# Performance work log

Hardware: AMD Instinct MI355X
Metric: run time of the kernel (lower is better)

Reference implementation:

```python
import jax, jax.numpy as jnp
import numpy as np

B, H, S, D = 2, 16, 2048, 64
NEG_BIG = -1e30  # stand-in for -inf; exp underflows to 0 identically in fp32


def setup_inputs() -> dict:
    key = jax.random.key(0)
    kq, kk, kv = jax.random.split(key, 3)
    q = jax.random.normal(kq, (B, H, S, D), dtype=jnp.float32)
    k = jax.random.normal(kk, (B, H, S, D), dtype=jnp.float32)
    v = jax.random.normal(kv, (B, H, S, D), dtype=jnp.float32)
    # causal mask, True = attend (matches masked_fill_(mask.logical_not(), -inf))
    mask = jnp.tril(jnp.ones((S, S), dtype=bool))[None, None]  # [1,1,S,S]
    return {"q": q, "k": k, "v": v, "mask": mask}


def reference(q, k, v, mask):
    # scaled dot-product attention: softmax(q k^T / sqrt(d)) v
    scale = q.shape[-1] ** -0.5
    weight = jnp.einsum("bhqd,bhkd->bhqk", q * scale, k)  # [B,H,S,S]
    weight = jnp.where(mask, weight, NEG_BIG)
    score = jax.nn.softmax(weight, axis=-1)  # stable: single max-subtract
    attn = jnp.einsum("bhqk,bhkd->bhqd", score, v)  # [B,H,S,D]
    return attn
```

## Files before the change

### kernel.cpp

```cpp
#include <hip/hip_runtime.h>

#define S_ 2048
#define D_ 64

typedef __bf16 bf16x2v __attribute__((ext_vector_type(2)));
typedef __bf16 bf16x8 __attribute__((ext_vector_type(8)));
typedef float f32x2 __attribute__((ext_vector_type(2)));
typedef float f32x4 __attribute__((ext_vector_type(4)));
typedef float f32x16 __attribute__((ext_vector_type(16)));
typedef unsigned uint4v __attribute__((ext_vector_type(4)));

#define QSCALE 0.180336880f

__device__ __forceinline__ unsigned cvtpk(float lo, float hi) {
    bf16x2v w; w[0] = (__bf16)lo; w[1] = (__bf16)hi;
    return __builtin_bit_cast(unsigned, w);
}

__device__ __forceinline__ float fexp2(float x) { return __builtin_amdgcn_exp2f(x); }

__device__ __forceinline__ int kap(int r) {
    return (r & ~12) | ((r & 4) << 1) | ((r & 8) >> 1);
}

__global__ __launch_bounds__(512, 2)
void fa_fwd(const float* __restrict__ qg, const float* __restrict__ kg,
            const float* __restrict__ vg, float* __restrict__ og) {
    __shared__ __attribute__((aligned(16))) __bf16 K_lds[2][2][64 * 64];
    __shared__ __attribute__((aligned(16))) __bf16 V_lds[2][2][64 * 64];
    __shared__ __attribute__((aligned(16))) float  mrg[9216];

    const int tid  = threadIdx.x;
    const int lane = tid & 63;
    const int wv   = tid >> 6;
    const int g    = wv >> 2;
    const int wq   = wv & 3;
    const int cq   = lane & 31;
    const int h    = lane >> 5;
    const int up   = wq & 1;

    const int bid = blockIdx.x;
    const int s   = bid >> 5;
    const int bh  = ((bid & 7) << 2) | ((bid >> 3) & 3);

    const size_t base = (size_t)bh * (S_ * D_);
    const float* Q = qg + base;
    const float* K = kg + base;
    const float* V = vg + base;
    float*       O = og + base;

    const int stid = tid & 255;
    const int kk   = stid >> 2;
    const int kd   = (stid & 3) * 16;
    const int vd2  = (stid & 31) * 2;
    const int vk8  = (stid >> 5) * 8;
    const int kp   = (kk & 32) | kap(kk & 31);
    const unsigned swq = (unsigned)((cq & 7) << 4);
    const int slot = (wq * 64 + lane) * 36;

    f32x4 rk[4];
    f32x2 rv2[8];

    auto loadtile = [&](int t) {
        const int kv0 = t * 64;
        const float* Kp = K + (size_t)(kv0 + kk) * D_ + kd;
        #pragma unroll
        for (int i = 0; i < 4; ++i) rk[i] = *(const f32x4*)(Kp + 4 * i);
        const float* Vp = V + (size_t)(kv0 + vk8) * D_ + vd2;
        #pragma unroll
        for (int i = 0; i < 8; ++i) rv2[i] = *(const f32x2*)(Vp + (size_t)i * D_);
    };

    auto writetile = [&](int buf) {
        const unsigned swzk = (unsigned)((kp & 7) << 4);
        bf16x8 w0, w1;
        #pragma unroll
        for (int j = 0; j < 4; ++j) {
            w0[j]     = (__bf16)rk[0][j];
            w0[4 + j] = (__bf16)rk[1][j];
            w1[j]     = (__bf16)rk[2][j];
            w1[4 + j] = (__bf16)rk[3][j];
        }
        *(bf16x8*)(&K_lds[g][buf][kp * 64 + ((((unsigned)(2 * kd)) ^ swzk) >> 1)])      = w0;
        *(bf16x8*)(&K_lds[g][buf][kp * 64 + ((((unsigned)(2 * kd + 16)) ^ swzk) >> 1)]) = w1;
        #pragma unroll
        for (int j = 0; j < 2; ++j) {
            const int d = vd2 + j;
            bf16x8 wt;
            #pragma unroll
            for (int i = 0; i < 8; ++i) wt[i] = (__bf16)rv2[i][j];
            *(bf16x8*)(&V_lds[g][buf][d * 64 + ((((unsigned)(2 * vk8)) ^ ((unsigned)((d & 7) << 4))) >> 1)]) = wt;
        }
    };

    for (int pass = 0; pass < 2; ++pass) {
        const int qt    = pass ? s : (15 - s);
        const int q0w   = qt * 128 + wq * 32;
        const int tdiag = 2 * qt + (wq >> 1);
        const int tbase = g ? (qt + 1) : 0;
        const int niter = qt + 1;

        bf16x8 qf[4];
        {
            const float* Qr = Q + (size_t)(q0w + cq) * D_;
            #pragma unroll
            for (int c = 0; c < 4; ++c) {
                const int d0 = c * 16 + h * 8;
                f32x4 a = *(const f32x4*)(Qr + d0);
                f32x4 b = *(const f32x4*)(Qr + d0 + 4);
                bf16x8 f;
                #pragma unroll
                for (int j = 0; j < 4; ++j) {
                    f[j]     = (__bf16)(a[j] * QSCALE);
                    f[4 + j] = (__bf16)(b[j] * QSCALE);
                }
                qf[c] = f;
            }
        }

        f32x16 acc0, acc1;
        #pragma unroll
        for (int i = 0; i < 16; ++i) { acc0[i] = 0.f; acc1[i] = 0.f; }
        float l_r = 0.f;

        auto compute = [&](int t, int buf) {
            const bool diag  = (t == tdiag);
            const bool do_s1 = !diag || up;
            const bool mask0 = diag && !up;
            const bool mask1 = diag && up;

            f32x16 s0, s1;
            #pragma unroll
            for (int i = 0; i < 16; ++i) { s0[i] = 0.f; s1[i] = 0.f; }
            __builtin_amdgcn_s_setprio(1);
            #pragma unroll
            for (int c = 0; c < 4; ++c) {
                const unsigned co = (unsigned)(c * 32 + h * 16);
                bf16x8 a0 = *(const bf16x8*)(&K_lds[g][buf][cq * 64 + ((co ^ swq) >> 1)]);
                s0 = __builtin_amdgcn_mfma_f32_32x32x16_bf16(a0, qf[c], s0, 0, 0, 0);
            }
            if (do_s1) {
                #pragma unroll
                for (int c = 0; c < 4; ++c) {
                    const unsigned co = (unsigned)(c * 32 + h * 16);
                    bf16x8 a1 = *(const bf16x8*)(&K_lds[g][buf][(32 + cq) * 64 + ((co ^ swq) >> 1)]);
                    s1 = __builtin_amdgcn_mfma_f32_32x32x16_bf16(a1, qf[c], s1, 0, 0, 0);
                }
            }
            __builtin_amdgcn_s_setprio(0);

            if (mask0) {
                #pragma unroll
                for (int reg = 0; reg < 16; ++reg)
                    if ((reg + (reg & 8) + 8 * h) > cq) s0[reg] = -1e30f;
            }
            if (mask1) {
                #pragma unroll
                for (int reg = 0; reg < 16; ++reg)
                    if ((reg + (reg & 8) + 8 * h) > cq) s1[reg] = -1e30f;
            }

            float ps0 = 0.f, ps1 = 0.f, ps2 = 0.f, ps3 = 0.f;
            #pragma unroll
            for (int gg = 0; gg < 4; ++gg) {
                s0[4 * gg]     = fexp2(s0[4 * gg]);     ps0 += s0[4 * gg];
                s0[4 * gg + 1] = fexp2(s0[4 * gg + 1]); ps1 += s0[4 * gg + 1];
                s0[4 * gg + 2] = fexp2(s0[4 * gg + 2]); ps2 += s0[4 * gg + 2];
                s0[4 * gg + 3] = fexp2(s0[4 * gg + 3]); ps3 += s0[4 * gg + 3];
            }
            if (do_s1) {
                #pragma unroll
                for (int gg = 0; gg < 4; ++gg) {
                    s1[4 * gg]     = fexp2(s1[4 * gg]);     ps0 += s1[4 * gg];
                    s1[4 * gg + 1] = fexp2(s1[4 * gg + 1]); ps1 += s1[4 * gg + 1];
                    s1[4 * gg + 2] = fexp2(s1[4 * gg + 2]); ps2 += s1[4 * gg + 2];
                    s1[4 * gg + 3] = fexp2(s1[4 * gg + 3]); ps3 += s1[4 * gg + 3];
                }
            }
            l_r += (ps0 + ps1) + (ps2 + ps3);

            __builtin_amdgcn_s_setprio(1);
            #pragma unroll
            for (int ks = 0; ks < 2; ++ks) {
                uint4v pw;
                #pragma unroll
                for (int j = 0; j < 4; ++j)
                    pw[j] = cvtpk(s0[8 * ks + 2 * j], s0[8 * ks + 2 * j + 1]);
                bf16x8 pb = __builtin_bit_cast(bf16x8, pw);
                const unsigned co = (unsigned)(ks * 32 + h * 16);
                bf16x8 va0 = *(const bf16x8*)(&V_lds[g][buf][cq * 64 + ((co ^ swq) >> 1)]);
                bf16x8 va1 = *(const bf16x8*)(&V_lds[g][buf][(32 + cq) * 64 + ((co ^ swq) >> 1)]);
                acc0 = __builtin_amdgcn_mfma_f32_32x32x16_bf16(va0, pb, acc0, 0, 0, 0);
                acc1 = __builtin_amdgcn_mfma_f32_32x32x16_bf16(va1, pb, acc1, 0, 0, 0);
            }
            if (do_s1) {
                #pragma unroll
                for (int ks = 0; ks < 2; ++ks) {
                    uint4v pw;
                    #pragma unroll
                    for (int j = 0; j < 4; ++j)
                        pw[j] = cvtpk(s1[8 * ks + 2 * j], s1[8 * ks + 2 * j + 1]);
                    bf16x8 pb = __builtin_bit_cast(bf16x8, pw);
                    const unsigned co = (unsigned)((ks + 2) * 32 + h * 16);
                    bf16x8 va0 = *(const bf16x8*)(&V_lds[g][buf][cq * 64 + ((co ^ swq) >> 1)]);
                    bf16x8 va1 = *(const bf16x8*)(&V_lds[g][buf][(32 + cq) * 64 + ((co ^ swq) >> 1)]);
                    acc0 = __builtin_amdgcn_mfma_f32_32x32x16_bf16(va0, pb, acc0, 0, 0, 0);
                    acc1 = __builtin_amdgcn_mfma_f32_32x32x16_bf16(va1, pb, acc1, 0, 0, 0);
                }
            }
            __builtin_amdgcn_s_setprio(0);
        };

        loadtile(tbase);
        for (int i = 0; i < niter; ++i) {
            const int buf = i & 1;
            writetile(buf);
            const bool more = (i + 1 < niter);
            f32x4 nk0, nk1, nk2, nk3;
            f32x2 nv0, nv1, nv2, nv3, nv4, nv5, nv6, nv7;
            if (more) {
                const int kv0 = (tbase + i + 1) * 64;
                const float* Kp = K + (size_t)(kv0 + kk) * D_ + kd;
                nk0 = *(const f32x4*)(Kp);
                nk1 = *(const f32x4*)(Kp + 4);
                nk2 = *(const f32x4*)(Kp + 8);
                nk3 = *(const f32x4*)(Kp + 12);
                const float* Vp = V + (size_t)(kv0 + vk8) * D_ + vd2;
                nv0 = *(const f32x2*)(Vp);
                nv1 = *(const f32x2*)(Vp + (size_t)1 * D_);
                nv2 = *(const f32x2*)(Vp + (size_t)2 * D_);
                nv3 = *(const f32x2*)(Vp + (size_t)3 * D_);
                nv4 = *(const f32x2*)(Vp + (size_t)4 * D_);
                nv5 = *(const f32x2*)(Vp + (size_t)5 * D_);
                nv6 = *(const f32x2*)(Vp + (size_t)6 * D_);
                nv7 = *(const f32x2*)(Vp + (size_t)7 * D_);
            }
            __syncthreads();
            const int t = tbase + i;
            if (t <= tdiag) compute(t, buf);
            if (more) {
                rk[0] = nk0; rk[1] = nk1; rk[2] = nk2; rk[3] = nk3;
                rv2[0] = nv0; rv2[1] = nv1; rv2[2] = nv2; rv2[3] = nv3;
                rv2[4] = nv4; rv2[5] = nv5; rv2[6] = nv6; rv2[7] = nv7;
            }
        }

        const float lt = l_r + __shfl_xor(l_r, 32);
        __syncthreads();
        if (g == 1) {
            mrg[slot] = lt;
            #pragma unroll
            for (int i = 0; i < 4; ++i) {
                f32x4 a, b;
                #pragma unroll
                for (int j = 0; j < 4; ++j) { a[j] = acc0[4 * i + j]; b[j] = acc1[4 * i + j]; }
                *(f32x4*)(&mrg[slot + 4 + 4 * i])  = a;
                *(f32x4*)(&mrg[slot + 20 + 4 * i]) = b;
            }
        }
        __syncthreads();
        if (g == 0) {
            const float lb = mrg[slot];
            const float inv = 1.0f / (lt + lb);
            float* Or = O + (size_t)(q0w + cq) * D_;
            #pragma unroll
            for (int rq = 0; rq < 4; ++rq) {
                f32x4 pa = *(const f32x4*)(&mrg[slot + 4 + 4 * rq]);
                f32x4 pb = *(const f32x4*)(&mrg[slot + 20 + 4 * rq]);
                f32x4 w0, w1;
                #pragma unroll
                for (int i = 0; i < 4; ++i) {
                    w0[i] = (acc0[4 * rq + i] + pa[i]) * inv;
                    w1[i] = (acc1[4 * rq + i] + pb[i]) * inv;
                }
                *(f32x4*)(Or + 8 * rq + 4 * h)      = w0;
                *(f32x4*)(Or + 32 + 8 * rq + 4 * h) = w1;
            }
        }
        __syncthreads();
    }
}

extern "C" void kernel_launch(void* const* d_in, const int* in_sizes, int n_in,
                              void* d_out, int out_size, void* d_ws, size_t ws_size,
                              hipStream_t stream) {
    const float* q = (const float*)d_in[0];
    const float* k = (const float*)d_in[1];
    const float* v = (const float*)d_in[2];
    float* out = (float*)d_out;
    dim3 grid(256, 1, 1);
    dim3 block(512, 1, 1);
    fa_fwd<<<grid, block, 0, stream>>>(q, k, v, out);
}
```

Measured before the change: 40.71 us.

## Process KV tiles in pairs per barrier and alias merge buffer onto LDS

After: 42.43 us. +4.2%, slower.

```diff
diff --git a/kernel.cpp b/kernel.cpp
--- a/kernel.cpp
+++ b/kernel.cpp
@@ -26,9 +26,8 @@
 __global__ __launch_bounds__(512, 2)
 void fa_fwd(const float* __restrict__ qg, const float* __restrict__ kg,
             const float* __restrict__ vg, float* __restrict__ og) {
-    __shared__ __attribute__((aligned(16))) __bf16 K_lds[2][2][64 * 64];
-    __shared__ __attribute__((aligned(16))) __bf16 V_lds[2][2][64 * 64];
-    __shared__ __attribute__((aligned(16))) float  mrg[9216];
+    __shared__ __attribute__((aligned(16))) __bf16 K_lds[2][2][2][64 * 64];
+    __shared__ __attribute__((aligned(16))) __bf16 V_lds[2][2][2][64 * 64];
 
     const int tid  = threadIdx.x;
     const int lane = tid & 63;
@@ -58,10 +57,10 @@
     const unsigned swq = (unsigned)((cq & 7) << 4);
     const int slot = (wq * 64 + lane) * 36;
 
-    f32x4 rk[4];
-    f32x2 rv2[8];
-
-    auto loadtile = [&](int t) {
+    f32x4 rkA[4], rkB[4];
+    f32x2 rvA[8], rvB[8];
+
+    auto loadsub = [&](f32x4* rk, f32x2* rv2, int t) {
         const int kv0 = t * 64;
         const float* Kp = K + (size_t)(kv0 + kk) * D_ + kd;
         #pragma unroll
@@ -71,7 +70,9 @@
         for (int i = 0; i < 8; ++i) rv2[i] = *(const f32x2*)(Vp + (size_t)i * D_);
     };
 
-    auto writetile = [&](int buf) {
+    auto writesub = [&](const f32x4* rk, const f32x2* rv2, int buf, int hh) {
+        __bf16* Kb = &K_lds[g][buf][hh][0];
+        __bf16* Vb = &V_lds[g][buf][hh][0];
         const unsigned swzk = (unsigned)((kp & 7) << 4);
         bf16x8 w0, w1;
         #pragma unroll
@@ -81,15 +82,15 @@
             w1[j]     = (__bf16)rk[2][j];
             w1[4 + j] = (__bf16)rk[3][j];
         }
-        *(bf16x8*)(&K_lds[g][buf][kp * 64 + ((((unsigned)(2 * kd)) ^ swzk) >> 1)])      = w0;
-        *(bf16x8*)(&K_lds[g][buf][kp * 64 + ((((unsigned)(2 * kd + 16)) ^ swzk) >> 1)]) = w1;
+        *(bf16x8*)(&Kb[kp * 64 + ((((unsigned)(2 * kd)) ^ swzk) >> 1)])      = w0;
+        *(bf16x8*)(&Kb[kp * 64 + ((((unsigned)(2 * kd + 16)) ^ swzk) >> 1)]) = w1;
         #pragma unroll
         for (int j = 0; j < 2; ++j) {
             const int d = vd2 + j;
             bf16x8 wt;
             #pragma unroll
             for (int i = 0; i < 8; ++i) wt[i] = (__bf16)rv2[i][j];
-            *(bf16x8*)(&V_lds[g][buf][d * 64 + ((((unsigned)(2 * vk8)) ^ ((unsigned)((d & 7) << 4))) >> 1)]) = wt;
+            *(bf16x8*)(&Vb[d * 64 + ((((unsigned)(2 * vk8)) ^ ((unsigned)((d & 7) << 4))) >> 1)]) = wt;
         }
     };
 
@@ -99,6 +100,7 @@
         const int tdiag = 2 * qt + (wq >> 1);
         const int tbase = g ? (qt + 1) : 0;
         const int niter = qt + 1;
+        const int npair = (niter + 1) >> 1;
 
         bf16x8 qf[4];
         {
@@ -123,7 +125,9 @@
         for (int i = 0; i < 16; ++i) { acc0[i] = 0.f; acc1[i] = 0.f; }
         float l_r = 0.f;
 
-        auto compute = [&](int t, int buf) {
+        auto compute = [&](int t, int buf, int hh) {
+            const __bf16* Kb = &K_lds[g][buf][hh][0];
+            const __bf16* Vb = &V_lds[g][buf][hh][0];
             const bool diag  = (t == tdiag);
             const bool do_s1 = !diag || up;
             const bool mask0 = diag && !up;
@@ -136,14 +140,14 @@
             #pragma unroll
             for (int c = 0; c < 4; ++c) {
                 const unsigned co = (unsigned)(c * 32 + h * 16);
-                bf16x8 a0 = *(const bf16x8*)(&K_lds[g][buf][cq * 64 + ((co ^ swq) >> 1)]);
+                bf16x8 a0 = *(const bf16x8*)(&Kb[cq * 64 + ((co ^ swq) >> 1)]);
                 s0 = __builtin_amdgcn_mfma_f32_32x32x16_bf16(a0, qf[c], s0, 0, 0, 0);
             }
             if (do_s1) {
                 #pragma unroll
                 for (int c = 0; c < 4; ++c) {
                     const unsigned co = (unsigned)(c * 32 + h * 16);
-                    bf16x8 a1 = *(const bf16x8*)(&K_lds[g][buf][(32 + cq) * 64 + ((co ^ swq) >> 1)]);
+                    bf16x8 a1 = *(const bf16x8*)(&Kb[(32 + cq) * 64 + ((co ^ swq) >> 1)]);
                     s1 = __builtin_amdgcn_mfma_f32_32x32x16_bf16(a1, qf[c], s1, 0, 0, 0);
                 }
             }
@@ -188,8 +192,8 @@
                     pw[j] = cvtpk(s0[8 * ks + 2 * j], s0[8 * ks + 2 * j + 1]);
                 bf16x8 pb = __builtin_bit_cast(bf16x8, pw);
                 const unsigned co = (unsigned)(ks * 32 + h * 16);
-                bf16x8 va0 = *(const bf16x8*)(&V_lds[g][buf][cq * 64 + ((co ^ swq) >> 1)]);
-                bf16x8 va1 = *(const bf16x8*)(&V_lds[g][buf][(32 + cq) * 64 + ((co ^ swq) >> 1)]);
+                bf16x8 va0 = *(const bf16x8*)(&Vb[cq * 64 + ((co ^ swq) >> 1)]);
+                bf16x8 va1 = *(const bf16x8*)(&Vb[(32 + cq) * 64 + ((co ^ swq) >> 1)]);
                 acc0 = __builtin_amdgcn_mfma_f32_32x32x16_bf16(va0, pb, acc0, 0, 0, 0);
                 acc1 = __builtin_amdgcn_mfma_f32_32x32x16_bf16(va1, pb, acc1, 0, 0, 0);
             }
@@ -202,8 +206,8 @@
                         pw[j] = cvtpk(s1[8 * ks + 2 * j], s1[8 * ks + 2 * j + 1]);
                     bf16x8 pb = __builtin_bit_cast(bf16x8, pw);
                     const unsigned co = (unsigned)((ks + 2) * 32 + h * 16);
-                    bf16x8 va0 = *(const bf16x8*)(&V_lds[g][buf][cq * 64 + ((co ^ swq) >> 1)]);
-                    bf16x8 va1 = *(const bf16x8*)(&V_lds[g][buf][(32 + cq) * 64 + ((co ^ swq) >> 1)]);
+                    bf16x8 va0 = *(const bf16x8*)(&Vb[cq * 64 + ((co ^ swq) >> 1)]);
+                    bf16x8 va1 = *(const bf16x8*)(&Vb[(32 + cq) * 64 + ((co ^ swq) >> 1)]);
                     acc0 = __builtin_amdgcn_mfma_f32_32x32x16_bf16(va0, pb, acc0, 0, 0, 0);
                     acc1 = __builtin_amdgcn_mfma_f32_32x32x16_bf16(va1, pb, acc1, 0, 0, 0);
                 }
@@ -211,42 +215,26 @@
             __builtin_amdgcn_s_setprio(0);
         };
 
-        loadtile(tbase);
-        for (int i = 0; i < niter; ++i) {
-            const int buf = i & 1;
-            writetile(buf);
-            const bool more = (i + 1 < niter);
-            f32x4 nk0, nk1, nk2, nk3;
-            f32x2 nv0, nv1, nv2, nv3, nv4, nv5, nv6, nv7;
-            if (more) {
-                const int kv0 = (tbase + i + 1) * 64;
-                const float* Kp = K + (size_t)(kv0 + kk) * D_ + kd;
-                nk0 = *(const f32x4*)(Kp);
-                nk1 = *(const f32x4*)(Kp + 4);
-                nk2 = *(const f32x4*)(Kp + 8);
-                nk3 = *(const f32x4*)(Kp + 12);
-                const float* Vp = V + (size_t)(kv0 + vk8) * D_ + vd2;
-                nv0 = *(const f32x2*)(Vp);
-                nv1 = *(const f32x2*)(Vp + (size_t)1 * D_);
-                nv2 = *(const f32x2*)(Vp + (size_t)2 * D_);
-                nv3 = *(const f32x2*)(Vp + (size_t)3 * D_);
-                nv4 = *(const f32x2*)(Vp + (size_t)4 * D_);
-                nv5 = *(const f32x2*)(Vp + (size_t)5 * D_);
-                nv6 = *(const f32x2*)(Vp + (size_t)6 * D_);
-                nv7 = *(const f32x2*)(Vp + (size_t)7 * D_);
-            }
+        {
+            loadsub(rkA, rvA, tbase);
+            if (niter > 1) loadsub(rkB, rvB, tbase + 1);
+        }
+        for (int p = 0; p < npair; ++p) {
+            const int buf = p & 1;
+            const int tA = tbase + 2 * p;
+            const bool hasB = (2 * p + 1 < niter);
+            writesub(rkA, rvA, buf, 0);
+            if (hasB) writesub(rkB, rvB, buf, 1);
             __syncthreads();
-            const int t = tbase + i;
-            if (t <= tdiag) compute(t, buf);
-            if (more) {
-                rk[0] = nk0; rk[1] = nk1; rk[2] = nk2; rk[3] = nk3;
-                rv2[0] = nv0; rv2[1] = nv1; rv2[2] = nv2; rv2[3] = nv3;
-                rv2[4] = nv4; rv2[5] = nv5; rv2[6] = nv6; rv2[7] = nv7;
-            }
+            if (2 * p + 2 < niter) loadsub(rkA, rvA, tbase + 2 * p + 2);
+            if (2 * p + 3 < niter) loadsub(rkB, rvB, tbase + 2 * p + 3);
+            if (tA <= tdiag) compute(tA, buf, 0);
+            if (hasB && (tA + 1 <= tdiag)) compute(tA + 1, buf, 1);
         }
 
         const float lt = l_r + __shfl_xor(l_r, 32);
         __syncthreads();
+        float* mrg = (float*)&K_lds[0][0][0][0];
         if (g == 1) {
             mrg[slot] = lt;
             #pragma unroll
```
